# Kernel tuning notes

Measured on AMD Instinct MI355X. Metric: run time of the kernel, lower is better.

The kernel has to match this reference:

```python
import jax, jax.numpy as jnp
import numpy as np

B, T, C, H = 2, 2048, 1024, 16
HD = C // H  # head dim = 64


def setup_inputs() -> dict:
    key = jax.random.key(0)
    ks = jax.random.split(key, 5)
    s = 1.0 / np.sqrt(C)
    return {
        "x": jax.random.normal(ks[0], (B, T, C), dtype=jnp.float32),
        "Wq": jax.random.normal(ks[1], (C, C), dtype=jnp.float32) * s,
        "bq": jnp.zeros((C,), dtype=jnp.float32),
        "Wk": jax.random.normal(ks[2], (C, C), dtype=jnp.float32) * s,
        "bk": jnp.zeros((C,), dtype=jnp.float32),
        "Wv": jax.random.normal(ks[3], (C, C), dtype=jnp.float32) * s,
        "bv": jnp.zeros((C,), dtype=jnp.float32),
        "Wp": jax.random.normal(ks[4], (C, C), dtype=jnp.float32) * s,
        "bp": jnp.zeros((C,), dtype=jnp.float32),
    }


def reference(x, Wq, bq, Wk, bk, Wv, bv, Wp, bp):
    # QKV projections -> [B, H, T, HD]
    def proj(W, b):
        return (x @ W.T + b).reshape(B, T, H, HD).transpose(0, 2, 1, 3)

    q = proj(Wq, bq)
    k = proj(Wk, bk)
    v = proj(Wv, bv)

    scale = 1.0 / np.sqrt(HD)
    att = jnp.einsum("bhtd,bhsd->bhts", q, k) * scale  # [B,H,T,T]
    causal = jnp.tril(jnp.ones((T, T), dtype=bool))
    att = jnp.where(causal, att, -jnp.inf)
    att = jax.nn.softmax(att, axis=-1)
    y = jnp.einsum("bhts,bhsd->bhtd", att, v)          # [B,H,T,HD]
    y = y.transpose(0, 2, 1, 3).reshape(B, T, C)
    return y @ Wp.T + bp
```

## Files before the change

### kernel.cpp

```cpp
#include <hip/hip_runtime.h>
#include <hip/hip_bf16.h>

#define BB 2
#define TT 2048
#define CC 1024
#define HH 16
#define HDD 64

typedef __attribute__((ext_vector_type(8))) short bf16x8;
typedef __attribute__((ext_vector_type(4))) float f32x4;

static __device__ __forceinline__ unsigned short f2bf(float f) {
  union { float f; unsigned u; } v; v.f = f;
  unsigned r = v.u + 0x7fffu + ((v.u >> 16) & 1u);
  return (unsigned short)(r >> 16);
}

static __device__ __forceinline__ unsigned fbits(float f) {
  union { float f; unsigned u; } v; v.f = f; return v.u;
}

static __device__ __forceinline__ unsigned pk_trunc(float lo, float hi) {
  return __builtin_amdgcn_perm(fbits(hi), fbits(lo), 0x07060302u);
}

static __device__ __forceinline__ float fexp2(float x) {
#if __has_builtin(__builtin_amdgcn_exp2f)
  return __builtin_amdgcn_exp2f(x);
#else
  return exp2f(x);
#endif
}

static __device__ __forceinline__ void gload_lds16(const unsigned short* g, unsigned short* l) {
  __builtin_amdgcn_global_load_lds((const __attribute__((address_space(1))) void*)g,
                                   (__attribute__((address_space(3))) void*)l, 16, 0, 0);
}

__global__ __launch_bounds__(256) void convert_all(
    const float* __restrict__ x, const float* __restrict__ Wq,
    const float* __restrict__ Wk, const float* __restrict__ Wv,
    const float* __restrict__ Wp, unsigned short* __restrict__ dst)
{
  const size_t M4 = 4194304, M1 = 1048576;
  const size_t e = ((size_t)blockIdx.x * 256 + threadIdx.x) * 8;
  const float* src; size_t off;
  if (e < M4)            { src = x;  off = e; }
  else if (e < M4 + M1)  { src = Wq; off = e - M4; }
  else if (e < M4 + 2*M1){ src = Wk; off = e - M4 - M1; }
  else if (e < M4 + 3*M1){ src = Wv; off = e - M4 - 2*M1; }
  else                   { src = Wp; off = e - M4 - 3*M1; }
  float4 a = *(const float4*)(src + off);
  float4 c = *(const float4*)(src + off + 4);
  unsigned short buf[8] = {f2bf(a.x), f2bf(a.y), f2bf(a.z), f2bf(a.w),
                           f2bf(c.x), f2bf(c.y), f2bf(c.z), f2bf(c.w)};
  *(uint4*)(dst + e) = *(const uint4*)buf;
}


__global__ __launch_bounds__(256) void gemm_mfma(
    const unsigned short* __restrict__ A, const unsigned short* __restrict__ W,
    const float* __restrict__ b0, const float* __restrict__ b1, const float* __restrict__ b2,
    unsigned short* __restrict__ oQ, unsigned short* __restrict__ oK,
    unsigned short* __restrict__ oVt)
{
  __shared__ unsigned short As[3][128][32];
  __shared__ unsigned short Bs[3][128][32];
  const int t = threadIdx.x;
  const int wv = __builtin_amdgcn_readfirstlane(t >> 6);
  const int ln = t & 63;
  const int l16 = ln & 15;
  const int quad = ln >> 4;
  const int mBase = blockIdx.x * 128;
  const int nBase = blockIdx.y * 128;
  const int wm = (wv >> 1) * 64, wn = (wv & 1) * 64;

  f32x4 acc[4][4];
#pragma unroll
  for (int i = 0; i < 4; i++)
#pragma unroll
    for (int j = 0; j < 4; j++) acc[i][j] = (f32x4){0.f, 0.f, 0.f, 0.f};

  const int rloc = t >> 2;
  const int csrc = ((t & 3) ^ ((t >> 3) & 3)) * 8;
  const unsigned short* gA = A + (size_t)(mBase + rloc) * CC + csrc;
  const unsigned short* gB = W + (size_t)(nBase + rloc) * CC + csrc;
  const int sw = (quad ^ ((l16 >> 1) & 3)) * 8;

#define STAGE(b, kt)                                                       \
  do {                                                                     \
    const size_t ko = (size_t)(kt) * 32;                                   \
    gload_lds16(gA + ko,           &As[b][0][0] + t * 8);                  \
    gload_lds16(gA + ko + 64 * CC, &As[b][64][0] + t * 8);                 \
    gload_lds16(gB + ko,           &Bs[b][0][0] + t * 8);                  \
    gload_lds16(gB + ko + 64 * CC, &Bs[b][64][0] + t * 8);                 \
  } while (0)

  STAGE(0, 0);
  STAGE(1, 1);
  int cur = 0, nxt2 = 2;
  for (int kt = 0; kt < 32; ++kt) {
    if (kt < 30) {
      STAGE(nxt2, kt + 2);
      asm volatile("s_waitcnt vmcnt(8)" ::: "memory");
    } else if (kt == 30) {
      asm volatile("s_waitcnt vmcnt(4)" ::: "memory");
    } else {
      asm volatile("s_waitcnt vmcnt(0)" ::: "memory");
    }
    __builtin_amdgcn_s_barrier();
    asm volatile("" ::: "memory");
    bf16x8 af[4], bfr[4];
#pragma unroll
    for (int i = 0; i < 4; ++i) af[i] = *(const bf16x8*)&As[cur][wm + i * 16 + l16][sw];
#pragma unroll
    for (int j = 0; j < 4; ++j) bfr[j] = *(const bf16x8*)&Bs[cur][wn + j * 16 + l16][sw];
    __builtin_amdgcn_s_setprio(1);
#pragma unroll
    for (int i = 0; i < 4; ++i)
#pragma unroll
      for (int j = 0; j < 4; ++j)
        acc[i][j] = __builtin_amdgcn_mfma_f32_16x16x32_bf16(af[i], bfr[j], acc[i][j], 0, 0, 0);
    __builtin_amdgcn_s_setprio(0);
    asm volatile("" ::: "memory");
    __builtin_amdgcn_s_barrier();
    asm volatile("" ::: "memory");
    cur = (cur == 2) ? 0 : cur + 1;
    nxt2 = (nxt2 == 2) ? 0 : nxt2 + 1;
  }
#undef STAGE

  const int which = nBase >> 10;
  const float* bias = which == 0 ? b0 : (which == 1 ? b1 : b2);
  unsigned short* dst = which == 0 ? oQ : (which == 1 ? oK : oVt);
  const float scl = which == 0 ? 0.1803368801f : 1.0f;
#pragma unroll
  for (int i = 0; i < 4; i++)
#pragma unroll
    for (int r = 0; r < 4; r++) {
      const int m = mBase + wm + i * 16 + quad * 4 + r;
      const int b = m >> 11, tp = m & 2047;
#pragma unroll
      for (int j = 0; j < 4; j++) {
        const int n = nBase + wn + j * 16 + l16;
        const int nl = n & 1023, h = nl >> 6, d = nl & 63;
        const unsigned short v = f2bf((acc[i][j][r] + bias[nl]) * scl);
        if (which < 2) dst[((size_t)(b * HH + h) * TT + tp) * HDD + d] = v;
        else           dst[((size_t)(b * HH + h) * HDD + d) * TT + tp] = v;
      }
    }
}

__global__ __launch_bounds__(512) void gemm_proj(
    const unsigned short* __restrict__ A, const unsigned short* __restrict__ W,
    const float* __restrict__ bias, float* __restrict__ out)
{
  __shared__ unsigned short As[3][128][32];
  __shared__ unsigned short Bs[3][128][32];
  const int t = threadIdx.x;
  const int wv = __builtin_amdgcn_readfirstlane(t >> 6);
  const int ln = t & 63;
  const int l16 = ln & 15;
  const int quad = ln >> 4;
  const int mBase = blockIdx.x * 128;
  const int nBase = blockIdx.y * 128;
  const int wm = (wv >> 2) * 64;
  const int wn = (wv & 3) * 32;

  f32x4 acc[4][2];
#pragma unroll
  for (int i = 0; i < 4; i++)
#pragma unroll
    for (int j = 0; j < 2; j++) acc[i][j] = (f32x4){0.f, 0.f, 0.f, 0.f};

  const int rloc = t >> 2;
  const int csrc = ((t & 3) ^ ((t >> 3) & 3)) * 8;
  const unsigned short* gA = A + (size_t)(mBase + rloc) * CC + csrc;
  const unsigned short* gB = W + (size_t)(nBase + rloc) * CC + csrc;
  const int sw = (quad ^ ((l16 >> 1) & 3)) * 8;

#define STAGE(b, kt)                                                       \
  do {                                                                     \
    const size_t ko = (size_t)(kt) * 32;                                   \
    gload_lds16(gA + ko, &As[b][0][0] + t * 8);                            \
    gload_lds16(gB + ko, &Bs[b][0][0] + t * 8);                            \
  } while (0)

  STAGE(0, 0);
  STAGE(1, 1);
  int cur = 0, nxt2 = 2;
  for (int kt = 0; kt < 32; ++kt) {
    if (kt < 30) {
      STAGE(nxt2, kt + 2);
      asm volatile("s_waitcnt vmcnt(4)" ::: "memory");
    } else if (kt == 30) {
      asm volatile("s_waitcnt vmcnt(2)" ::: "memory");
    } else {
      asm volatile("s_waitcnt vmcnt(0)" ::: "memory");
    }
    __builtin_amdgcn_s_barrier();
    asm volatile("" ::: "memory");
    bf16x8 af[4], bfr[2];
#pragma unroll
    for (int i = 0; i < 4; ++i) af[i] = *(const bf16x8*)&As[cur][wm + i * 16 + l16][sw];
#pragma unroll
    for (int j = 0; j < 2; ++j) bfr[j] = *(const bf16x8*)&Bs[cur][wn + j * 16 + l16][sw];
    __builtin_amdgcn_s_setprio(1);
#pragma unroll
    for (int i = 0; i < 4; ++i)
#pragma unroll
      for (int j = 0; j < 2; ++j)
        acc[i][j] = __builtin_amdgcn_mfma_f32_16x16x32_bf16(af[i], bfr[j], acc[i][j], 0, 0, 0);
    __builtin_amdgcn_s_setprio(0);
    asm volatile("" ::: "memory");
    __builtin_amdgcn_s_barrier();
    asm volatile("" ::: "memory");
    cur = (cur == 2) ? 0 : cur + 1;
    nxt2 = (nxt2 == 2) ? 0 : nxt2 + 1;
  }
#undef STAGE

#pragma unroll
  for (int i = 0; i < 4; i++)
#pragma unroll
    for (int r = 0; r < 4; r++) {
      const int m = mBase + wm + i * 16 + quad * 4 + r;
#pragma unroll
      for (int j = 0; j < 2; j++) {
        const int n = nBase + wn + j * 16 + l16;
        out[(size_t)m * CC + n] = acc[i][j][r] + bias[n];
      }
    }
}

__global__ __launch_bounds__(256, 2) void attn_mfma(
    const unsigned short* __restrict__ Q, const unsigned short* __restrict__ K,
    const unsigned short* __restrict__ Vt, unsigned short* __restrict__ y)
{
  __shared__ unsigned short QP[128][72];
  __shared__ unsigned short Ks[2][64][72];
  __shared__ unsigned short Vts[2][64][72];

  const int t = threadIdx.x;
  const int a = blockIdx.x;
  const int bh = blockIdx.y;
  const int wave = t >> 6;
  const int lane = t & 63;
  const int l16 = lane & 15;
  const int quad = lane >> 4;

  const size_t base = (size_t)bh * TT * HDD;
  const int qtL = a, qtH = 31 - a;
  const int qBaseL = qtL * 64, qBaseH = qtH * 64;

#pragma unroll
  for (int p = 0; p < 4; p++) {
    const int c = p * 256 + t;
    const int r = c >> 3, off = (c & 7) * 8;
    const int srcRow = (r < 64) ? (qBaseL + r) : (qBaseH + r - 64);
    *(uint4*)&QP[r][off] = *(const uint4*)(Q + base + (size_t)srcRow * HDD + off);
  }

  const int sr = t >> 2, sc = (t & 3) * 8;
  const unsigned short* kbase = K + base + (size_t)sr * HDD + sc;
  const unsigned short* vbase = Vt + base + (size_t)sr * TT + sc;
  uint4 kr0 = *(const uint4*)(kbase);
  uint4 kr1 = *(const uint4*)(kbase + 32);
  uint4 vr0 = *(const uint4*)(vbase);
  uint4 vr1 = *(const uint4*)(vbase + 32);
  __syncthreads();

  bf16x8 qfL0 = *(const bf16x8*)&QP[wave * 16 + l16][quad * 8];
  bf16x8 qfL1 = *(const bf16x8*)&QP[wave * 16 + l16][32 + quad * 8];
  bf16x8 qfH0 = *(const bf16x8*)&QP[64 + wave * 16 + l16][quad * 8];
  bf16x8 qfH1 = *(const bf16x8*)&QP[64 + wave * 16 + l16][32 + quad * 8];
  unsigned short (*PtH)[72] = (unsigned short (*)[72])&QP[wave * 16];
  unsigned short (*PtL)[72] = (unsigned short (*)[72])&QP[64 + wave * 16];

  float lL = 0.f, lH = 0.f;
  f32x4 OfrL[4], OfrH[4];
#pragma unroll
  for (int dt = 0; dt < 4; dt++) {
    OfrL[dt] = (f32x4){0.f, 0.f, 0.f, 0.f};
    OfrH[dt] = (f32x4){0.f, 0.f, 0.f, 0.f};
  }

  for (int kt = 0; kt <= qtH; kt++) {
    const int buf = kt & 1;
    *(uint4*)&Ks[buf][sr][sc]       = kr0;
    *(uint4*)&Ks[buf][sr][sc + 32]  = kr1;
    *(uint4*)&Vts[buf][sr][sc]      = vr0;
    *(uint4*)&Vts[buf][sr][sc + 32] = vr1;
    __syncthreads();
    if (kt < qtH) {
      kr0 = *(const uint4*)(kbase + (size_t)(kt + 1) * 64 * HDD);
      kr1 = *(const uint4*)(kbase + (size_t)(kt + 1) * 64 * HDD + 32);
      vr0 = *(const uint4*)(vbase + (kt + 1) * 64);
      vr1 = *(const uint4*)(vbase + (kt + 1) * 64 + 32);
    }
    const bool doLo = (kt <= qtL);

    f32x4 StH[4], StL[4];
#pragma unroll
    for (int ct = 0; ct < 4; ct++) {
      bf16x8 a0 = *(const bf16x8*)&Ks[buf][ct * 16 + l16][quad * 8];
      bf16x8 a1 = *(const bf16x8*)&Ks[buf][ct * 16 + l16][32 + quad * 8];
      f32x4 s = (f32x4){0.f, 0.f, 0.f, 0.f};
      s = __builtin_amdgcn_mfma_f32_16x16x32_bf16(a0, qfH0, s, 0, 0, 0);
      s = __builtin_amdgcn_mfma_f32_16x16x32_bf16(a1, qfH1, s, 0, 0, 0);
      StH[ct] = s;
      if (doLo) {
        f32x4 s2 = (f32x4){0.f, 0.f, 0.f, 0.f};
        s2 = __builtin_amdgcn_mfma_f32_16x16x32_bf16(a0, qfL0, s2, 0, 0, 0);
        s2 = __builtin_amdgcn_mfma_f32_16x16x32_bf16(a1, qfL1, s2, 0, 0, 0);
        StL[ct] = s2;
      }
    }

    if (kt == qtH) {
#pragma unroll
      for (int ct = 0; ct < 4; ct++) {
        float p[4];
#pragma unroll
        for (int r = 0; r < 4; r++) {
          float pv = fexp2(StH[ct][r]);
          if (ct * 16 + quad * 4 + r > wave * 16 + l16) pv = 0.f;
          p[r] = pv;
        }
        lH += (p[0] + p[1]) + (p[2] + p[3]);
        uint2 pk = {pk_trunc(p[0], p[1]), pk_trunc(p[2], p[3])};
        *(uint2*)&PtH[l16][ct * 16 + quad * 4] = pk;
      }
    } else {
#pragma unroll
      for (int ct = 0; ct < 4; ct++) {
        float p[4];
#pragma unroll
        for (int r = 0; r < 4; r++) p[r] = fexp2(StH[ct][r]);
        lH += (p[0] + p[1]) + (p[2] + p[3]);
        uint2 pk = {pk_trunc(p[0], p[1]), pk_trunc(p[2], p[3])};
        *(uint2*)&PtH[l16][ct * 16 + quad * 4] = pk;
      }
    }
    if (doLo) {
      if (kt == qtL) {
#pragma unroll
        for (int ct = 0; ct < 4; ct++) {
          float p[4];
#pragma unroll
          for (int r = 0; r < 4; r++) {
            float pv = fexp2(StL[ct][r]);
            if (ct * 16 + quad * 4 + r > wave * 16 + l16) pv = 0.f;
            p[r] = pv;
          }
          lL += (p[0] + p[1]) + (p[2] + p[3]);
          uint2 pk = {pk_trunc(p[0], p[1]), pk_trunc(p[2], p[3])};
          *(uint2*)&PtL[l16][ct * 16 + quad * 4] = pk;
        }
      } else {
#pragma unroll
        for (int ct = 0; ct < 4; ct++) {
          float p[4];
#pragma unroll
          for (int r = 0; r < 4; r++) p[r] = fexp2(StL[ct][r]);
          lL += (p[0] + p[1]) + (p[2] + p[3]);
          uint2 pk = {pk_trunc(p[0], p[1]), pk_trunc(p[2], p[3])};
          *(uint2*)&PtL[l16][ct * 16 + quad * 4] = pk;
        }
      }
    }

    bf16x8 paH0 = *(const bf16x8*)&PtH[l16][quad * 8];
    bf16x8 paH1 = *(const bf16x8*)&PtH[l16][32 + quad * 8];
    bf16x8 paL0, paL1;
    if (doLo) {
      paL0 = *(const bf16x8*)&PtL[l16][quad * 8];
      paL1 = *(const bf16x8*)&PtL[l16][32 + quad * 8];
    }
#pragma unroll
    for (int dt = 0; dt < 4; dt++) {
      bf16x8 vb0 = *(const bf16x8*)&Vts[buf][dt * 16 + l16][quad * 8];
      bf16x8 vb1 = *(const bf16x8*)&Vts[buf][dt * 16 + l16][32 + quad * 8];
      OfrH[dt] = __builtin_amdgcn_mfma_f32_16x16x32_bf16(paH0, vb0, OfrH[dt], 0, 0, 0);
      OfrH[dt] = __builtin_amdgcn_mfma_f32_16x16x32_bf16(paH1, vb1, OfrH[dt], 0, 0, 0);
      if (doLo) {
        OfrL[dt] = __builtin_amdgcn_mfma_f32_16x16x32_bf16(paL0, vb0, OfrL[dt], 0, 0, 0);
        OfrL[dt] = __builtin_amdgcn_mfma_f32_16x16x32_bf16(paL1, vb1, OfrL[dt], 0, 0, 0);
      }
    }
  }

  lL += __shfl_xor(lL, 16, 64); lL += __shfl_xor(lL, 32, 64);
  lH += __shfl_xor(lH, 16, 64); lH += __shfl_xor(lH, 32, 64);

  const int b = bh >> 4, h = bh & 15;
  float lRowL[4], lRowH[4];
#pragma unroll
  for (int r = 0; r < 4; r++) {
    lRowL[r] = __shfl(lL, quad * 4 + r, 16);
    lRowH[r] = __shfl(lH, quad * 4 + r, 16);
  }
#pragma unroll
  for (int r = 0; r < 4; r++) {
    const int qL = qBaseL + wave * 16 + quad * 4 + r;
    const int qH = qBaseH + wave * 16 + quad * 4 + r;
    const float invL = 1.0f / lRowL[r];
    const float invH = 1.0f / lRowH[r];
    unsigned short* ypL = y + ((size_t)(b * TT + qL)) * CC + h * 64 + l16;
    unsigned short* ypH = y + ((size_t)(b * TT + qH)) * CC + h * 64 + l16;
#pragma unroll
    for (int dt = 0; dt < 4; dt++) {
      ypL[dt * 16] = f2bf(OfrL[dt][r] * invL);
      ypH[dt * 16] = f2bf(OfrH[dt][r] * invH);
    }
  }
}

extern "C" void kernel_launch(void* const* d_in, const int* in_sizes, int n_in,
                              void* d_out, int out_size, void* d_ws, size_t ws_size,
                              hipStream_t stream) {
  const float* x  = (const float*)d_in[0];
  const float* Wq = (const float*)d_in[1];
  const float* bq = (const float*)d_in[2];
  const float* Wk = (const float*)d_in[3];
  const float* bk = (const float*)d_in[4];
  const float* Wv = (const float*)d_in[5];
  const float* bv = (const float*)d_in[6];
  const float* Wp = (const float*)d_in[7];
  const float* bp = (const float*)d_in[8];

  const size_t M4 = 4194304, M1 = 1048576;
  unsigned short* xb   = (unsigned short*)d_ws;
  unsigned short* wqb  = xb + M4;
  unsigned short* wpb  = wqb + 3 * M1;
  unsigned short* wsQ  = wpb + M1;
  unsigned short* wsK  = wsQ + M4;
  unsigned short* wsVt = wsK + M4;
  unsigned short* yb   = wsVt + M4;

  convert_all<<<4096, 256, 0, stream>>>(x, Wq, Wk, Wv, Wp, xb);
  gemm_mfma<<<dim3(32, 24), 256, 0, stream>>>(xb, wqb, bq, bk, bv,
                                              wsQ, wsK, wsVt);
  attn_mfma<<<dim3(16, BB * HH), 256, 0, stream>>>(wsQ, wsK, wsVt, yb);
  gemm_proj<<<dim3(32, 8), 512, 0, stream>>>(yb, wpb, bp, (float*)d_out);
}
```

Baseline: 186.3 us.

## Split attention low/high query tiles across separate waves with 512-thread blocks

The attention kernel now launches 512 threads per block. Waves 0-3 handle the low query tile and waves 4-7 the high tile, where before each wave processed both. Q fragments are loaded straight from global memory instead of staged through shared memory, and each thread loads one K/V chunk per tile instead of two. This halves per-wave register pressure and doubles the waves available to hide latency. The trade-off is that low-tile waves sit idle at the barriers once their causal range ends, since every wave keeps iterating up to the high tile.

```diff
diff --git a/kernel.cpp b/kernel.cpp
--- a/kernel.cpp
+++ b/kernel.cpp
@@ -57,7 +57,6 @@
   *(uint4*)(dst + e) = *(const uint4*)buf;
 }
 
-
 __global__ __launch_bounds__(256) void gemm_mfma(
     const unsigned short* __restrict__ A, const unsigned short* __restrict__ W,
     const float* __restrict__ b0, const float* __restrict__ b1, const float* __restrict__ b2,
@@ -233,11 +232,11 @@
     }
 }
 
-__global__ __launch_bounds__(256, 2) void attn_mfma(
+__global__ __launch_bounds__(512, 4) void attn_mfma(
     const unsigned short* __restrict__ Q, const unsigned short* __restrict__ K,
     const unsigned short* __restrict__ Vt, unsigned short* __restrict__ y)
 {
-  __shared__ unsigned short QP[128][72];
+  __shared__ unsigned short Pt[128][72];
   __shared__ unsigned short Ks[2][64][72];
   __shared__ unsigned short Vts[2][64][72];
 
@@ -251,168 +250,99 @@
 
   const size_t base = (size_t)bh * TT * HDD;
   const int qtL = a, qtH = 31 - a;
-  const int qBaseL = qtL * 64, qBaseH = qtH * 64;
-
-#pragma unroll
-  for (int p = 0; p < 4; p++) {
-    const int c = p * 256 + t;
-    const int r = c >> 3, off = (c & 7) * 8;
-    const int srcRow = (r < 64) ? (qBaseL + r) : (qBaseH + r - 64);
-    *(uint4*)&QP[r][off] = *(const uint4*)(Q + base + (size_t)srcRow * HDD + off);
-  }
-
-  const int sr = t >> 2, sc = (t & 3) * 8;
+  const bool isHi = wave >= 4;
+  const int myQt = isHi ? qtH : qtL;
+  const int myQBase = (isHi ? qtH : qtL) * 64;
+  const int rowInTile = (wave & 3) * 16 + l16;
+
+  const unsigned short* qrow = Q + base + (size_t)(myQBase + rowInTile) * HDD + quad * 8;
+  bf16x8 qf0 = *(const bf16x8*)(qrow);
+  bf16x8 qf1 = *(const bf16x8*)(qrow + 32);
+
+  unsigned short (*Ptw)[72] = (unsigned short (*)[72])&Pt[wave * 16];
+
+  const int sr = t >> 3, sc = (t & 7) * 8;
   const unsigned short* kbase = K + base + (size_t)sr * HDD + sc;
   const unsigned short* vbase = Vt + base + (size_t)sr * TT + sc;
-  uint4 kr0 = *(const uint4*)(kbase);
-  uint4 kr1 = *(const uint4*)(kbase + 32);
-  uint4 vr0 = *(const uint4*)(vbase);
-  uint4 vr1 = *(const uint4*)(vbase + 32);
-  __syncthreads();
-
-  bf16x8 qfL0 = *(const bf16x8*)&QP[wave * 16 + l16][quad * 8];
-  bf16x8 qfL1 = *(const bf16x8*)&QP[wave * 16 + l16][32 + quad * 8];
-  bf16x8 qfH0 = *(const bf16x8*)&QP[64 + wave * 16 + l16][quad * 8];
-  bf16x8 qfH1 = *(const bf16x8*)&QP[64 + wave * 16 + l16][32 + quad * 8];
-  unsigned short (*PtH)[72] = (unsigned short (*)[72])&QP[wave * 16];
-  unsigned short (*PtL)[72] = (unsigned short (*)[72])&QP[64 + wave * 16];
-
-  float lL = 0.f, lH = 0.f;
-  f32x4 OfrL[4], OfrH[4];
-#pragma unroll
-  for (int dt = 0; dt < 4; dt++) {
-    OfrL[dt] = (f32x4){0.f, 0.f, 0.f, 0.f};
-    OfrH[dt] = (f32x4){0.f, 0.f, 0.f, 0.f};
-  }
+  uint4 kr = *(const uint4*)(kbase);
+  uint4 vr = *(const uint4*)(vbase);
+
+  float lsum = 0.f;
+  f32x4 Ofr[4];
+#pragma unroll
+  for (int dt = 0; dt < 4; dt++) Ofr[dt] = (f32x4){0.f, 0.f, 0.f, 0.f};
 
   for (int kt = 0; kt <= qtH; kt++) {
     const int buf = kt & 1;
-    *(uint4*)&Ks[buf][sr][sc]       = kr0;
-    *(uint4*)&Ks[buf][sr][sc + 32]  = kr1;
-    *(uint4*)&Vts[buf][sr][sc]      = vr0;
-    *(uint4*)&Vts[buf][sr][sc + 32] = vr1;
+    *(uint4*)&Ks[buf][sr][sc]  = kr;
+    *(uint4*)&Vts[buf][sr][sc] = vr;
     __syncthreads();
     if (kt < qtH) {
-      kr0 = *(const uint4*)(kbase + (size_t)(kt + 1) * 64 * HDD);
-      kr1 = *(const uint4*)(kbase + (size_t)(kt + 1) * 64 * HDD + 32);
-      vr0 = *(const uint4*)(vbase + (kt + 1) * 64);
-      vr1 = *(const uint4*)(vbase + (kt + 1) * 64 + 32);
-    }
-    const bool doLo = (kt <= qtL);
-
-    f32x4 StH[4], StL[4];
-#pragma unroll
-    for (int ct = 0; ct < 4; ct++) {
-      bf16x8 a0 = *(const bf16x8*)&Ks[buf][ct * 16 + l16][quad * 8];
-      bf16x8 a1 = *(const bf16x8*)&Ks[buf][ct * 16 + l16][32 + quad * 8];
-      f32x4 s = (f32x4){0.f, 0.f, 0.f, 0.f};
-      s = __builtin_amdgcn_mfma_f32_16x16x32_bf16(a0, qfH0, s, 0, 0, 0);
-      s = __builtin_amdgcn_mfma_f32_16x16x32_bf16(a1, qfH1, s, 0, 0, 0);
-      StH[ct] = s;
-      if (doLo) {
-        f32x4 s2 = (f32x4){0.f, 0.f, 0.f, 0.f};
-        s2 = __builtin_amdgcn_mfma_f32_16x16x32_bf16(a0, qfL0, s2, 0, 0, 0);
-        s2 = __builtin_amdgcn_mfma_f32_16x16x32_bf16(a1, qfL1, s2, 0, 0, 0);
-        StL[ct] = s2;
-      }
-    }
-
-    if (kt == qtH) {
+      kr = *(const uint4*)(kbase + (size_t)(kt + 1) * 64 * HDD);
+      vr = *(const uint4*)(vbase + (kt + 1) * 64);
+    }
+    if (kt <= myQt) {
+      f32x4 St[4];
 #pragma unroll
       for (int ct = 0; ct < 4; ct++) {
-        float p[4];
-#pragma unroll
-        for (int r = 0; r < 4; r++) {
-          float pv = fexp2(StH[ct][r]);
-          if (ct * 16 + quad * 4 + r > wave * 16 + l16) pv = 0.f;
-          p[r] = pv;
-        }
-        lH += (p[0] + p[1]) + (p[2] + p[3]);
-        uint2 pk = {pk_trunc(p[0], p[1]), pk_trunc(p[2], p[3])};
-        *(uint2*)&PtH[l16][ct * 16 + quad * 4] = pk;
-      }
-    } else {
-#pragma unroll
-      for (int ct = 0; ct < 4; ct++) {
-        float p[4];
-#pragma unroll
-        for (int r = 0; r < 4; r++) p[r] = fexp2(StH[ct][r]);
-        lH += (p[0] + p[1]) + (p[2] + p[3]);
-        uint2 pk = {pk_trunc(p[0], p[1]), pk_trunc(p[2], p[3])};
-        *(uint2*)&PtH[l16][ct * 16 + quad * 4] = pk;
-      }
-    }
-    if (doLo) {
-      if (kt == qtL) {
+        bf16x8 a0 = *(const bf16x8*)&Ks[buf][ct * 16 + l16][quad * 8];
+        bf16x8 a1 = *(const bf16x8*)&Ks[buf][ct * 16 + l16][32 + quad * 8];
+        f32x4 s = (f32x4){0.f, 0.f, 0.f, 0.f};
+        s = __builtin_amdgcn_mfma_f32_16x16x32_bf16(a0, qf0, s, 0, 0, 0);
+        s = __builtin_amdgcn_mfma_f32_16x16x32_bf16(a1, qf1, s, 0, 0, 0);
+        St[ct] = s;
+      }
+      if (kt == myQt) {
 #pragma unroll
         for (int ct = 0; ct < 4; ct++) {
           float p[4];
 #pragma unroll
           for (int r = 0; r < 4; r++) {
-            float pv = fexp2(StL[ct][r]);
-            if (ct * 16 + quad * 4 + r > wave * 16 + l16) pv = 0.f;
+            float pv = fexp2(St[ct][r]);
+            if (ct * 16 + quad * 4 + r > rowInTile) pv = 0.f;
             p[r] = pv;
           }
-          lL += (p[0] + p[1]) + (p[2] + p[3]);
+          lsum += (p[0] + p[1]) + (p[2] + p[3]);
           uint2 pk = {pk_trunc(p[0], p[1]), pk_trunc(p[2], p[3])};
-          *(uint2*)&PtL[l16][ct * 16 + quad * 4] = pk;
+          *(uint2*)&Ptw[l16][ct * 16 + quad * 4] = pk;
         }
       } else {
 #pragma unroll
         for (int ct = 0; ct < 4; ct++) {
           float p[4];
 #pragma unroll
-          for (int r = 0; r < 4; r++) p[r] = fexp2(StL[ct][r]);
-          lL += (p[0] + p[1]) + (p[2] + p[3]);
+          for (int r = 0; r < 4; r++) p[r] = fexp2(St[ct][r]);
+          lsum += (p[0] + p[1]) + (p[2] + p[3]);
           uint2 pk = {pk_trunc(p[0], p[1]), pk_trunc(p[2], p[3])};
-          *(uint2*)&PtL[l16][ct * 16 + quad * 4] = pk;
+          *(uint2*)&Ptw[l16][ct * 16 + quad * 4] = pk;
         }
       }
-    }
-
-    bf16x8 paH0 = *(const bf16x8*)&PtH[l16][quad * 8];
-    bf16x8 paH1 = *(const bf16x8*)&PtH[l16][32 + quad * 8];
-    bf16x8 paL0, paL1;
-    if (doLo) {
-      paL0 = *(const bf16x8*)&PtL[l16][quad * 8];
-      paL1 = *(const bf16x8*)&PtL[l16][32 + quad * 8];
-    }
-#pragma unroll
-    for (int dt = 0; dt < 4; dt++) {
-      bf16x8 vb0 = *(const bf16x8*)&Vts[buf][dt * 16 + l16][quad * 8];
-      bf16x8 vb1 = *(const bf16x8*)&Vts[buf][dt * 16 + l16][32 + quad * 8];
-      OfrH[dt] = __builtin_amdgcn_mfma_f32_16x16x32_bf16(paH0, vb0, OfrH[dt], 0, 0, 0);
-      OfrH[dt] = __builtin_amdgcn_mfma_f32_16x16x32_bf16(paH1, vb1, OfrH[dt], 0, 0, 0);
-      if (doLo) {
-        OfrL[dt] = __builtin_amdgcn_mfma_f32_16x16x32_bf16(paL0, vb0, OfrL[dt], 0, 0, 0);
-        OfrL[dt] = __builtin_amdgcn_mfma_f32_16x16x32_bf16(paL1, vb1, OfrL[dt], 0, 0, 0);
+      bf16x8 pa0 = *(const bf16x8*)&Ptw[l16][quad * 8];
+      bf16x8 pa1 = *(const bf16x8*)&Ptw[l16][32 + quad * 8];
+#pragma unroll
+      for (int dt = 0; dt < 4; dt++) {
+        bf16x8 vb0 = *(const bf16x8*)&Vts[buf][dt * 16 + l16][quad * 8];
+        bf16x8 vb1 = *(const bf16x8*)&Vts[buf][dt * 16 + l16][32 + quad * 8];
+        Ofr[dt] = __builtin_amdgcn_mfma_f32_16x16x32_bf16(pa0, vb0, Ofr[dt], 0, 0, 0);
+        Ofr[dt] = __builtin_amdgcn_mfma_f32_16x16x32_bf16(pa1, vb1, Ofr[dt], 0, 0, 0);
       }
     }
   }
 
-  lL += __shfl_xor(lL, 16, 64); lL += __shfl_xor(lL, 32, 64);
-  lH += __shfl_xor(lH, 16, 64); lH += __shfl_xor(lH, 32, 64);
+  lsum += __shfl_xor(lsum, 16, 64);
+  lsum += __shfl_xor(lsum, 32, 64);
 
   const int b = bh >> 4, h = bh & 15;
-  float lRowL[4], lRowH[4];
+  float lRow[4];
+#pragma unroll
+  for (int r = 0; r < 4; r++) lRow[r] = __shfl(lsum, quad * 4 + r, 16);
 #pragma unroll
   for (int r = 0; r < 4; r++) {
-    lRowL[r] = __shfl(lL, quad * 4 + r, 16);
-    lRowH[r] = __shfl(lH, quad * 4 + r, 16);
-  }
-#pragma unroll
-  for (int r = 0; r < 4; r++) {
-    const int qL = qBaseL + wave * 16 + quad * 4 + r;
-    const int qH = qBaseH + wave * 16 + quad * 4 + r;
-    const float invL = 1.0f / lRowL[r];
-    const float invH = 1.0f / lRowH[r];
-    unsigned short* ypL = y + ((size_t)(b * TT + qL)) * CC + h * 64 + l16;
-    unsigned short* ypH = y + ((size_t)(b * TT + qH)) * CC + h * 64 + l16;
-#pragma unroll
-    for (int dt = 0; dt < 4; dt++) {
-      ypL[dt * 16] = f2bf(OfrL[dt][r] * invL);
-      ypH[dt * 16] = f2bf(OfrH[dt][r] * invH);
-    }
+    const int q = myQBase + (wave & 3) * 16 + quad * 4 + r;
+    const float inv = 1.0f / lRow[r];
+    unsigned short* yp = y + ((size_t)(b * TT + q)) * CC + h * 64 + l16;
+#pragma unroll
+    for (int dt = 0; dt < 4; dt++) yp[dt * 16] = f2bf(Ofr[dt][r] * inv);
   }
 }
 
@@ -441,6 +371,6 @@
   convert_all<<<4096, 256, 0, stream>>>(x, Wq, Wk, Wv, Wp, xb);
   gemm_mfma<<<dim3(32, 24), 256, 0, stream>>>(xb, wqb, bq, bk, bv,
                                               wsQ, wsK, wsVt);
-  attn_mfma<<<dim3(16, BB * HH), 256, 0, stream>>>(wsQ, wsK, wsVt, yb);
+  attn_mfma<<<dim3(16, BB * HH), 512, 0, stream>>>(wsQ, wsK, wsVt, yb);
   gemm_proj<<<dim3(32, 8), 512, 0, stream>>>(yb, wpb, bp, (float*)d_out);
 }
```

Measured after the change: 183.7 us. Within noise of the previous version (-1.4%).
